# Optimization experiments

Hardware: AMD Instinct MI355X
Metric: run time of the kernel (lower is better)

Reference implementation:

```python
import jax, jax.numpy as jnp
import numpy as np

N, M, C = 4096, 1024, 64
KERNEL_SIZE = (0.1, 0.1)  # box extents; threshold is kernel_size/2 on |dx|,|dy|


def setup_inputs() -> dict:
    key = jax.random.key(0)
    k1, k2, k3 = jax.random.split(key, 3)
    values = jax.random.normal(k1, (N, C), dtype=jnp.float32)
    coords = jax.random.uniform(k2, (N, 2), dtype=jnp.float32)
    query_coords = jax.random.uniform(k3, (M, 2), dtype=jnp.float32)
    return {"values": values, "coords": coords, "query_coords": query_coords}


def reference(values, coords, query_coords):
    # shift buffer is (0,0) so no shift branch; box-kernel mask branch.
    kw, kh = KERNEL_SIZE
    diffs = query_coords[:, None, :] - coords[None, :, :]          # [M, N, 2]
    mask = (jnp.abs(diffs[..., 0]) < kw / 2) & (jnp.abs(diffs[..., 1]) < kh / 2)  # [M, N]
    neg = jnp.finfo(values.dtype).min
    # per-query masked max over points == ragged split + per-segment max in the original
    masked = jnp.where(mask[:, :, None], values[None, :, :], neg)  # [M, N, C]
    return jnp.max(masked, axis=1)                                  # [M, C]
```

## Files before the change

### kernel.cpp

```cpp
#include <hip/hip_runtime.h>

constexpr int N = 4096;
constexpr int M = 1024;
constexpr int C = 64;
constexpr int WAVES = 4;
constexpr int ITERS = N / (64 * WAVES);
#define HALF_KW 0.05f
#define NEG_INF (-3.402823466e38f)

__global__ __launch_bounds__(256) void maxpool_box_kernel(
    const float* __restrict__ values,
    const float* __restrict__ coords,
    const float* __restrict__ qcoords,
    float* __restrict__ out)
{
    const int q    = blockIdx.x;
    const int lane = threadIdx.x;
    const int w    = threadIdx.y;

    const float qx = qcoords[2 * q + 0];
    const float qy = qcoords[2 * q + 1];

    unsigned long long masks[ITERS];
    #pragma unroll
    for (int i = 0; i < ITERS; ++i) {
        const int j = w * 64 + i * (64 * WAVES) + lane;
        const float2 c = ((const float2*)coords)[j];
        const bool in = (fabsf(qx - c.x) < HALF_KW) &&
                        (fabsf(qy - c.y) < HALF_KW);
        masks[i] = __ballot(in);
    }

    float acc = NEG_INF;
    #pragma unroll 1
    for (int i = 0; i < ITERS; ++i) {
        unsigned long long m = masks[i];
        const int base = w * 64 + i * (64 * WAVES);
        while (m) {
            const int bit = __ffsll((unsigned long long)m) - 1;
            m &= (m - 1);
            const int p = base + bit;
            acc = fmaxf(acc, values[p * C + lane]);
        }
    }

    __shared__ float part[WAVES][C];
    part[w][lane] = acc;
    __syncthreads();
    if (w == 0) {
        const float r = fmaxf(fmaxf(part[0][lane], part[1][lane]),
                              fmaxf(part[2][lane], part[3][lane]));
        out[q * C + lane] = r;
    }
}

extern "C" void kernel_launch(void* const* d_in, const int* in_sizes, int n_in,
                              void* d_out, int out_size, void* d_ws, size_t ws_size,
                              hipStream_t stream) {
    const float* values  = (const float*)d_in[0];
    const float* coords  = (const float*)d_in[1];
    const float* qcoords = (const float*)d_in[2];
    float* out = (float*)d_out;

    dim3 block(64, WAVES);
    maxpool_box_kernel<<<M, block, 0, stream>>>(values, coords, qcoords, out);
}
```

Before: 65.49 us.

## Compact matching points into shared list and gather values with float4 loads

Matching point indices are written to a shared-memory list with atomics instead of per-wave ballot masks, so all four waves share the gather work evenly. Each wave then processes four points at once, with 16 lanes per point reading float4 values, and the 16 partial maxima are reduced in shared memory. Coordinate loads use float4 to test two points per thread. This adds 16KB of LDS per block and shared atomics, and the order of the list is nondeterministic, though max is order-independent.

```diff
diff --git a/kernel.cpp b/kernel.cpp
--- a/kernel.cpp
+++ b/kernel.cpp
@@ -3,8 +3,6 @@
 constexpr int N = 4096;
 constexpr int M = 1024;
 constexpr int C = 64;
-constexpr int WAVES = 4;
-constexpr int ITERS = N / (64 * WAVES);
 #define HALF_KW 0.05f
 #define NEG_INF (-3.402823466e38f)
 
@@ -14,43 +12,64 @@
     const float* __restrict__ qcoords,
     float* __restrict__ out)
 {
+    __shared__ int    s_cnt;
+    __shared__ int    s_list[N];
+    __shared__ float4 s_part[16][16];
+
     const int q    = blockIdx.x;
-    const int lane = threadIdx.x;
-    const int w    = threadIdx.y;
+    const int tid  = threadIdx.x;
+    const int lane = tid & 63;
+    const int w    = tid >> 6;
+
+    if (tid == 0) s_cnt = 0;
+    __syncthreads();
 
     const float qx = qcoords[2 * q + 0];
     const float qy = qcoords[2 * q + 1];
 
-    unsigned long long masks[ITERS];
+    const float4* c4p = (const float4*)coords;
     #pragma unroll
-    for (int i = 0; i < ITERS; ++i) {
-        const int j = w * 64 + i * (64 * WAVES) + lane;
-        const float2 c = ((const float2*)coords)[j];
-        const bool in = (fabsf(qx - c.x) < HALF_KW) &&
-                        (fabsf(qy - c.y) < HALF_KW);
-        masks[i] = __ballot(in);
+    for (int i = 0; i < N / (256 * 2); ++i) {
+        const int pair = i * 256 + tid;
+        const float4 cc = c4p[pair];
+        const bool in0 = (fabsf(qx - cc.x) < HALF_KW) && (fabsf(qy - cc.y) < HALF_KW);
+        const bool in1 = (fabsf(qx - cc.z) < HALF_KW) && (fabsf(qy - cc.w) < HALF_KW);
+        if (in0) { int k = atomicAdd(&s_cnt, 1); s_list[k] = 2 * pair; }
+        if (in1) { int k = atomicAdd(&s_cnt, 1); s_list[k] = 2 * pair + 1; }
     }
+    __syncthreads();
 
-    float acc = NEG_INF;
-    #pragma unroll 1
-    for (int i = 0; i < ITERS; ++i) {
-        unsigned long long m = masks[i];
-        const int base = w * 64 + i * (64 * WAVES);
-        while (m) {
-            const int bit = __ffsll((unsigned long long)m) - 1;
-            m &= (m - 1);
-            const int p = base + bit;
-            acc = fmaxf(acc, values[p * C + lane]);
+    const int cnt = s_cnt;
+    const int G   = (cnt + 3) >> 2;
+    if (cnt > 0 && tid < G * 4 - cnt) s_list[cnt + tid] = s_list[0];
+    __syncthreads();
+
+    const int sub = lane >> 4;
+    const int cq  = lane & 15;
+    const float4* v4 = (const float4*)values;
+    float4 acc = make_float4(NEG_INF, NEG_INF, NEG_INF, NEG_INF);
+    for (int g = w; g < G; g += 4) {
+        const int p = s_list[g * 4 + sub];
+        const float4 v = v4[p * 16 + cq];
+        acc.x = fmaxf(acc.x, v.x);
+        acc.y = fmaxf(acc.y, v.y);
+        acc.z = fmaxf(acc.z, v.z);
+        acc.w = fmaxf(acc.w, v.w);
+    }
+    s_part[w * 4 + sub][cq] = acc;
+    __syncthreads();
+
+    if (tid < 16) {
+        float4 r = s_part[0][tid];
+        #pragma unroll
+        for (int k = 1; k < 16; ++k) {
+            const float4 t = s_part[k][tid];
+            r.x = fmaxf(r.x, t.x);
+            r.y = fmaxf(r.y, t.y);
+            r.z = fmaxf(r.z, t.z);
+            r.w = fmaxf(r.w, t.w);
         }
-    }
-
-    __shared__ float part[WAVES][C];
-    part[w][lane] = acc;
-    __syncthreads();
-    if (w == 0) {
-        const float r = fmaxf(fmaxf(part[0][lane], part[1][lane]),
-                              fmaxf(part[2][lane], part[3][lane]));
-        out[q * C + lane] = r;
+        ((float4*)out)[q * 16 + tid] = r;
     }
 }
 
@@ -62,6 +81,5 @@
     const float* qcoords = (const float*)d_in[2];
     float* out = (float*)d_out;
 
-    dim3 block(64, WAVES);
-    maxpool_box_kernel<<<M, block, 0, stream>>>(values, coords, qcoords, out);
+    maxpool_box_kernel<<<M, 256, 0, stream>>>(values, coords, qcoords, out);
 }
```

After: 61.80 us. 5.6% less time.
